# Performance work log

Measured on AMD Instinct MI355X. Metric: run time of the kernel, lower is better.

The kernel has to match this reference:

```python
import jax, jax.numpy as jnp
from jax import lax
import numpy as np

MAX_VAL = 255.0
LEVELS = 5
MS_WEIGHTS = np.array([0.0448, 0.2856, 0.3001, 0.2363, 0.1333], dtype=np.float32)


def _gaussian_window(window_size: int, sigma: float) -> jnp.ndarray:
    # 1D gaussian -> outer product -> [1, 1, ws, ws] conv kernel (channel=1 depthwise)
    x = np.arange(window_size, dtype=np.float64)
    g = np.exp(-((x - window_size // 2) ** 2) / (2.0 * sigma ** 2))
    g = (g / g.sum()).astype(np.float32)
    w2d = np.outer(g, g)
    return jnp.asarray(w2d[None, None, :, :])


def _conv_same(x, win, pad):
    return lax.conv_general_dilated(
        x, win, window_strides=(1, 1), padding=[(pad, pad), (pad, pad)],
        dimension_numbers=('NCHW', 'OIHW', 'NCHW'))


def _ssim_level(img1, img2):
    _, _, w, h = img1.shape
    window_size = min(w, h, 11)
    sigma = 1.5 * window_size / 11
    win = _gaussian_window(window_size, sigma)
    pad = window_size // 2

    mu1 = _conv_same(img1, win, pad)
    mu2 = _conv_same(img2, win, pad)
    mu1_sq = mu1 * mu1
    mu2_sq = mu2 * mu2
    mu1_mu2 = mu1 * mu2
    sigma1_sq = _conv_same(img1 * img1, win, pad) - mu1_sq
    sigma2_sq = _conv_same(img2 * img2, win, pad) - mu2_sq
    sigma12 = _conv_same(img1 * img2, win, pad) - mu1_mu2

    C1 = (0.01 * MAX_VAL) ** 2
    C2 = (0.03 * MAX_VAL) ** 2
    V1 = 2.0 * sigma12 + C2
    V2 = sigma1_sq + sigma2_sq + C2
    ssim_map = (2.0 * mu1_mu2 + C1) * V1 / ((mu1_sq + mu2_sq + C1) * V2)
    mcs_map = V1 / V2
    return ssim_map.mean(), mcs_map.mean()


def _avg_pool2(x):
    b, c, h, w = x.shape
    return x.reshape(b, c, h // 2, 2, w // 2, 2).mean(axis=(3, 5))


def _ms_ssim(img1, img2):
    msssim = []
    mcs = []
    for _ in range(LEVELS):
        s, m = _ssim_level(img1, img2)
        msssim.append(s)
        mcs.append(m)
        img1 = _avg_pool2(img1)
        img2 = _avg_pool2(img2)
    weight = jnp.asarray(MS_WEIGHTS)
    mcs = jnp.stack(mcs)
    value = jnp.prod(mcs[:LEVELS - 1] ** weight[:LEVELS - 1]) * msssim[-1] ** weight[LEVELS - 1]
    return jnp.clip(value / 2.0, 0.0, 1.0)


def setup_inputs() -> dict:
    key = jax.random.key(0)
    k1, k2 = jax.random.split(key)
    shape = (16, 1, 512, 512)
    img1 = jax.random.uniform(k1, shape, dtype=jnp.float32)
    img2 = jax.random.uniform(k2, shape, dtype=jnp.float32)
    return {"img1": img1, "img2": img2}


def reference(img1, img2):
    return _ms_ssim(img1, img2)
```

## Files before the change

kernel.cpp:

```cpp
#include <hip/hip_runtime.h>
#include <math.h>


#define WS 11
#define TW 64
#define TH 32
#define SROWS 42
#define HSTRIDE 68

__device__ __forceinline__ void gauss_weights(float* w) {
    float s = 0.f;
#pragma unroll
    for (int j = 0; j < WS; ++j) {
        float d = (float)(j - 5);
        float e = expf(-d * d / 4.5f);
        w[j] = e;
        s += e;
    }
    float inv = 1.f / s;
#pragma unroll
    for (int j = 0; j < WS; ++j) w[j] *= inv;
}

__global__ __launch_bounds__(256) void pool_all_kernel(
    const float* __restrict__ img1, const float* __restrict__ img2,
    float* __restrict__ l1a, float* __restrict__ l1b,
    float* __restrict__ l2a, float* __restrict__ l2b,
    float* __restrict__ l3a, float* __restrict__ l3b,
    float* __restrict__ l4a, float* __restrict__ l4b)
{
    __shared__ float buf[64 * 68];
    __shared__ float pl1[32 * 36];
    __shared__ float pl2[16 * 20];
    __shared__ float pl3[8 * 12];
    const int tid = threadIdx.x;
    const int rx = blockIdx.x, ry = blockIdx.y, b = blockIdx.z;
    const int gx0 = rx * 64, gy0 = ry * 64;

#pragma unroll 1
    for (int q = 0; q < 2; ++q) {
        const float* src = (q == 0 ? img1 : img2) + (size_t)b * 512 * 512;
        float* d1 = (q == 0 ? l1a : l1b) + (size_t)b * 256 * 256;
        float* d2 = (q == 0 ? l2a : l2b) + (size_t)b * 128 * 128;
        float* d3 = (q == 0 ? l3a : l3b) + (size_t)b * 64 * 64;
        float* d4 = (q == 0 ? l4a : l4b) + (size_t)b * 32 * 32;
        if (q) __syncthreads();
        for (int t = tid; t < 1024; t += 256) {
            int r = t >> 4, c4 = t & 15;
            float4 v = *(const float4*)(src + (size_t)(gy0 + r) * 512 + gx0 + 4 * c4);
            *(float4*)&buf[r * 68 + 4 * c4] = v;
        }
        __syncthreads();
        for (int t = tid; t < 1024; t += 256) {
            int r = t >> 5, c = t & 31;
            const float* p = &buf[(2 * r) * 68 + 2 * c];
            float v = 0.25f * ((p[0] + p[1]) + (p[68] + p[69]));
            pl1[r * 36 + c] = v;
            d1[(size_t)(32 * ry + r) * 256 + 32 * rx + c] = v;
        }
        __syncthreads();
        {
            int r = tid >> 4, c = tid & 15;
            const float* p = &pl1[(2 * r) * 36 + 2 * c];
            float v = 0.25f * ((p[0] + p[1]) + (p[36] + p[37]));
            pl2[r * 20 + c] = v;
            d2[(size_t)(16 * ry + r) * 128 + 16 * rx + c] = v;
        }
        __syncthreads();
        if (tid < 64) {
            int r = tid >> 3, c = tid & 7;
            const float* p = &pl2[(2 * r) * 20 + 2 * c];
            float v = 0.25f * ((p[0] + p[1]) + (p[20] + p[21]));
            pl3[r * 12 + c] = v;
            d3[(size_t)(8 * ry + r) * 64 + 8 * rx + c] = v;
        }
        __syncthreads();
        if (tid < 16) {
            int r = tid >> 2, c = tid & 3;
            const float* p = &pl3[(2 * r) * 12 + 2 * c];
            float v = 0.25f * ((p[0] + p[1]) + (p[12] + p[13]));
            d4[(size_t)(4 * ry + r) * 32 + 4 * rx + c] = v;
        }
    }
}

__global__ __launch_bounds__(256) void ssim_fused_kernel(
    const float* __restrict__ img1, const float* __restrict__ img2,
    const float* __restrict__ l1a, const float* __restrict__ l1b,
    const float* __restrict__ l2a, const float* __restrict__ l2b,
    const float* __restrict__ l3a, const float* __restrict__ l3b,
    const float* __restrict__ l4a, const float* __restrict__ l4b,
    float* __restrict__ partials)
{
    __shared__ float hS[SROWS * HSTRIDE];
    __shared__ float hD[SROWS * HSTRIDE];
    __shared__ float hS2[SROWS * HSTRIDE];
    __shared__ float hD2[SROWS * HSTRIDE];
    __shared__ float red[2][4];

    const int tid = threadIdx.x;
    const int lin = blockIdx.x;

    int level, base;
    if (lin < 2048)      { level = 0; base = 0; }
    else if (lin < 2560) { level = 1; base = 2048; }
    else if (lin < 2688) { level = 2; base = 2560; }
    else if (lin < 2720) { level = 3; base = 2688; }
    else                 { level = 4; base = 2720; }
    const int Wt[5]   = {512, 256, 128, 64, 32};
    const int ntxl[5] = {3, 2, 1, 0, 0};
    const int ntyl[5] = {4, 3, 2, 1, 0};
    const int W = Wt[level], H = W;
    const int li = lin - base;
    const int tx = li & ((1 << ntxl[level]) - 1);
    const int rem = li >> ntxl[level];
    const int ty = rem & ((1 << ntyl[level]) - 1);
    const int b = rem >> ntyl[level];

    const float* ip1; const float* ip2;
    if (level == 0)      { ip1 = img1; ip2 = img2; }
    else if (level == 1) { ip1 = l1a; ip2 = l1b; }
    else if (level == 2) { ip1 = l2a; ip2 = l2b; }
    else if (level == 3) { ip1 = l3a; ip2 = l3b; }
    else                 { ip1 = l4a; ip2 = l4b; }
    const float* p1 = ip1 + (size_t)b * H * W;
    const float* p2 = ip2 + (size_t)b * H * W;

    const int x0 = tx * TW, y0 = ty * TH;

    float w[WS];
    gauss_weights(w);

#pragma unroll 1
    for (int t = tid; t < SROWS * 16; t += 256) {
        int r = t >> 4, xg = t & 15;
        int gy = y0 - 5 + r;
        int gxb = x0 - 8 + 4 * xg;
        float fs[20], fd[20];
        if (gy >= 0 && gy < H) {
            const float* r1p = p1 + (size_t)gy * W;
            const float* r2p = p2 + (size_t)gy * W;
#pragma unroll
            for (int k = 0; k < 5; ++k) {
                int gx = gxb + 4 * k;
                float4 a = make_float4(0.f, 0.f, 0.f, 0.f);
                float4 c = make_float4(0.f, 0.f, 0.f, 0.f);
                if (gx >= 0 && gx + 3 < W) {
                    a = *(const float4*)(r1p + gx);
                    c = *(const float4*)(r2p + gx);
                } else if (gx + 3 >= 0 && gx < W) {
                    float t1[4] = {0.f, 0.f, 0.f, 0.f};
                    float t2[4] = {0.f, 0.f, 0.f, 0.f};
#pragma unroll
                    for (int u = 0; u < 4; ++u) {
                        int gxx = gx + u;
                        if (gxx >= 0 && gxx < W) { t1[u] = r1p[gxx]; t2[u] = r2p[gxx]; }
                    }
                    a = make_float4(t1[0], t1[1], t1[2], t1[3]);
                    c = make_float4(t2[0], t2[1], t2[2], t2[3]);
                }
                fs[4 * k]     = a.x + c.x;  fd[4 * k]     = a.x - c.x;
                fs[4 * k + 1] = a.y + c.y;  fd[4 * k + 1] = a.y - c.y;
                fs[4 * k + 2] = a.z + c.z;  fd[4 * k + 2] = a.z - c.z;
                fs[4 * k + 3] = a.w + c.w;  fd[4 * k + 3] = a.w - c.w;
            }
        } else {
#pragma unroll
            for (int k = 0; k < 20; ++k) { fs[k] = 0.f; fd[k] = 0.f; }
        }
        float qs[14], qd[14];
#pragma unroll
        for (int k = 0; k < 14; ++k) {
            qs[k] = fs[k + 3] * fs[k + 3];
            qd[k] = fd[k + 3] * fd[k + 3];
        }
        float oS[4], oD[4], oS2[4], oD2[4];
#pragma unroll
        for (int c = 0; c < 4; ++c) {
            float aS = 0.f, aD = 0.f, aS2 = 0.f, aD2 = 0.f;
#pragma unroll
            for (int j = 0; j < WS; ++j) {
                float wj = w[j];
                aS  = fmaf(wj, fs[3 + c + j], aS);
                aD  = fmaf(wj, fd[3 + c + j], aD);
                aS2 = fmaf(wj, qs[c + j], aS2);
                aD2 = fmaf(wj, qd[c + j], aD2);
            }
            oS[c] = aS; oD[c] = aD; oS2[c] = aS2; oD2[c] = aD2;
        }
        int ho = r * HSTRIDE + 4 * xg;
        *(float4*)&hS[ho]  = make_float4(oS[0], oS[1], oS[2], oS[3]);
        *(float4*)&hD[ho]  = make_float4(oD[0], oD[1], oD[2], oD[3]);
        *(float4*)&hS2[ho] = make_float4(oS2[0], oS2[1], oS2[2], oS2[3]);
        *(float4*)&hD2[ho] = make_float4(oD2[0], oD2[1], oD2[2], oD2[3]);
    }
    __syncthreads();

    const int x = tid & 15;
    const int g = tid >> 4;
    float accS[2][4], accD[2][4], accS2[2][4], accD2[2][4];
#pragma unroll
    for (int rr = 0; rr < 2; ++rr)
#pragma unroll
        for (int c = 0; c < 4; ++c) {
            accS[rr][c] = 0.f; accD[rr][c] = 0.f;
            accS2[rr][c] = 0.f; accD2[rr][c] = 0.f;
        }

#pragma unroll
    for (int r = 0; r < 12; ++r) {
        int ho = (2 * g + r) * HSTRIDE + 4 * x;
        float4 vS  = *(const float4*)&hS[ho];
        float4 vD  = *(const float4*)&hD[ho];
        float4 vS2 = *(const float4*)&hS2[ho];
        float4 vD2 = *(const float4*)&hD2[ho];
        float lS[4] = {vS.x, vS.y, vS.z, vS.w};
        float lD[4] = {vD.x, vD.y, vD.z, vD.w};
        float lS2[4] = {vS2.x, vS2.y, vS2.z, vS2.w};
        float lD2[4] = {vD2.x, vD2.y, vD2.z, vD2.w};
        if (r < 11) {
            float wv = w[r];
#pragma unroll
            for (int c = 0; c < 4; ++c) {
                accS[0][c]  = fmaf(wv, lS[c],  accS[0][c]);
                accD[0][c]  = fmaf(wv, lD[c],  accD[0][c]);
                accS2[0][c] = fmaf(wv, lS2[c], accS2[0][c]);
                accD2[0][c] = fmaf(wv, lD2[c], accD2[0][c]);
            }
        }
        if (r >= 1) {
            float wv = w[r - 1];
#pragma unroll
            for (int c = 0; c < 4; ++c) {
                accS[1][c]  = fmaf(wv, lS[c],  accS[1][c]);
                accD[1][c]  = fmaf(wv, lD[c],  accD[1][c]);
                accS2[1][c] = fmaf(wv, lS2[c], accS2[1][c]);
                accD2[1][c] = fmaf(wv, lD2[c], accD2[1][c]);
            }
        }
    }

    const float C1 = 6.5025f;
    const float C2 = 58.5225f;
    const int Hv = min(TH, H - y0);
    const int Wv = min(TW, W - x0);
    float sacc = 0.f, macc = 0.f;
#pragma unroll
    for (int rr = 0; rr < 2; ++rr) {
        int row = 2 * g + rr;
#pragma unroll
        for (int c = 0; c < 4; ++c) {
            float ms = accS[rr][c], md = accD[rr][c];
            float es = accS2[rr][c], ed = accD2[rr][c];
            float ms2 = ms * ms, md2 = md * md;
            float a  = 0.5f * (ms2 - md2);
            float bb = 0.5f * (ms2 + md2);
            float pq = 0.5f * (es - ed);
            float qq = 0.5f * (es + ed);
            float V1 = (pq - a) + C2;
            float V2 = (qq - bb) + C2;
            float num = a + C1;
            float den = bb + C1;
            float inv = 1.0f / (den * V2);
            float sv = num * V1 * inv;
            float mv = V1 * den * inv;
            if (row < Hv && (4 * x + c) < Wv) { sacc += sv; macc += mv; }
        }
    }

#pragma unroll
    for (int o = 32; o > 0; o >>= 1) {
        sacc += __shfl_down(sacc, o);
        macc += __shfl_down(macc, o);
    }
    int wave = tid >> 6, lane = tid & 63;
    if (lane == 0) { red[0][wave] = sacc; red[1][wave] = macc; }
    __syncthreads();
    if (tid == 0) {
        float s = red[0][0] + red[0][1] + red[0][2] + red[0][3];
        float m = red[1][0] + red[1][1] + red[1][2] + red[1][3];
        partials[2 * lin] = s;
        partials[2 * lin + 1] = m;
    }
}

__global__ __launch_bounds__(256) void finalize_kernel(
    const float* __restrict__ partials, float* __restrict__ out)
{
    __shared__ float lvl_s[5], lvl_m[5];
    __shared__ float red[2][4];
    const int nb[5] = {2048, 512, 128, 32, 16};
    const int off[5] = {0, 2048, 2560, 2688, 2720};
    const float npix[5] = {16.f * 512 * 512, 16.f * 256 * 256, 16.f * 128 * 128,
                           16.f * 64 * 64, 16.f * 32 * 32};
    const int tid = threadIdx.x;

    for (int l = 0; l < 5; ++l) {
        float s = 0.f, m = 0.f;
        for (int i = tid; i < nb[l]; i += 256) {
            s += partials[2 * (off[l] + i)];
            m += partials[2 * (off[l] + i) + 1];
        }
#pragma unroll
        for (int o = 32; o > 0; o >>= 1) {
            s += __shfl_down(s, o);
            m += __shfl_down(m, o);
        }
        int wave = tid >> 6, lane = tid & 63;
        if (lane == 0) { red[0][wave] = s; red[1][wave] = m; }
        __syncthreads();
        if (tid == 0) {
            lvl_s[l] = (red[0][0] + red[0][1] + red[0][2] + red[0][3]) / npix[l];
            lvl_m[l] = (red[1][0] + red[1][1] + red[1][2] + red[1][3]) / npix[l];
        }
        __syncthreads();
    }

    if (tid == 0) {
        const float w[5] = {0.0448f, 0.2856f, 0.3001f, 0.2363f, 0.1333f};
        float v = powf(lvl_m[0], w[0]) * powf(lvl_m[1], w[1]) * powf(lvl_m[2], w[2]) *
                  powf(lvl_m[3], w[3]) * powf(lvl_s[4], w[4]);
        v *= 0.5f;
        v = fminf(fmaxf(v, 0.f), 1.f);
        out[0] = v;
    }
}

extern "C" void kernel_launch(void* const* d_in, const int* in_sizes, int n_in,
                              void* d_out, int out_size, void* d_ws, size_t ws_size,
                              hipStream_t stream) {
    const float* img1 = (const float*)d_in[0];
    const float* img2 = (const float*)d_in[1];
    float* out = (float*)d_out;

    const int B = 16;

    float* wsf = (float*)d_ws;
    float* partials = wsf;
    float* p = wsf + 5472;
    float* l1a = p; p += (size_t)B * 256 * 256;
    float* l1b = p; p += (size_t)B * 256 * 256;
    float* l2a = p; p += (size_t)B * 128 * 128;
    float* l2b = p; p += (size_t)B * 128 * 128;
    float* l3a = p; p += (size_t)B * 64 * 64;
    float* l3b = p; p += (size_t)B * 64 * 64;
    float* l4a = p; p += (size_t)B * 32 * 32;
    float* l4b = p; p += (size_t)B * 32 * 32;

    dim3 block(256);

    pool_all_kernel<<<dim3(8, 8, B), block, 0, stream>>>(
        img1, img2, l1a, l1b, l2a, l2b, l3a, l3b, l4a, l4b);

    ssim_fused_kernel<<<dim3(2736), block, 0, stream>>>(
        img1, img2, l1a, l1b, l2a, l2b, l3a, l3b, l4a, l4b, partials);

    finalize_kernel<<<1, block, 0, stream>>>(partials, out);
}
```

Measured before the change: 129.4 us.

## Fuse image pyramid pooling into level-0 SSIM kernel and split remaining levels

Removes the standalone pooling kernel. The level-0 SSIM tile kernel now also computes the 2x2 average pools for levels 1–4 from its own 64x32 tile and writes them to global buffers. The remaining levels run in a separate kernel that reads those buffers. This avoids a second full pass over both input images and one launch, at the cost of more work and shared memory in the level-0 kernel. Levels 1–4 can no longer overlap with level 0, since they now run in a later launch.

```diff
diff --git a/kernel.cpp b/kernel.cpp
--- a/kernel.cpp
+++ b/kernel.cpp
@@ -22,114 +22,13 @@
     for (int j = 0; j < WS; ++j) w[j] *= inv;
 }
 
-__global__ __launch_bounds__(256) void pool_all_kernel(
-    const float* __restrict__ img1, const float* __restrict__ img2,
-    float* __restrict__ l1a, float* __restrict__ l1b,
-    float* __restrict__ l2a, float* __restrict__ l2b,
-    float* __restrict__ l3a, float* __restrict__ l3b,
-    float* __restrict__ l4a, float* __restrict__ l4b)
+__device__ __forceinline__ void ssim_tile(
+    const float* __restrict__ p1, const float* __restrict__ p2,
+    int H, int W, int x0, int y0, const float* w,
+    float* hS, float* hD, float* hS2, float* hD2,
+    float red[2][4], float* __restrict__ partials, int part_idx)
 {
-    __shared__ float buf[64 * 68];
-    __shared__ float pl1[32 * 36];
-    __shared__ float pl2[16 * 20];
-    __shared__ float pl3[8 * 12];
     const int tid = threadIdx.x;
-    const int rx = blockIdx.x, ry = blockIdx.y, b = blockIdx.z;
-    const int gx0 = rx * 64, gy0 = ry * 64;
-
-#pragma unroll 1
-    for (int q = 0; q < 2; ++q) {
-        const float* src = (q == 0 ? img1 : img2) + (size_t)b * 512 * 512;
-        float* d1 = (q == 0 ? l1a : l1b) + (size_t)b * 256 * 256;
-        float* d2 = (q == 0 ? l2a : l2b) + (size_t)b * 128 * 128;
-        float* d3 = (q == 0 ? l3a : l3b) + (size_t)b * 64 * 64;
-        float* d4 = (q == 0 ? l4a : l4b) + (size_t)b * 32 * 32;
-        if (q) __syncthreads();
-        for (int t = tid; t < 1024; t += 256) {
-            int r = t >> 4, c4 = t & 15;
-            float4 v = *(const float4*)(src + (size_t)(gy0 + r) * 512 + gx0 + 4 * c4);
-            *(float4*)&buf[r * 68 + 4 * c4] = v;
-        }
-        __syncthreads();
-        for (int t = tid; t < 1024; t += 256) {
-            int r = t >> 5, c = t & 31;
-            const float* p = &buf[(2 * r) * 68 + 2 * c];
-            float v = 0.25f * ((p[0] + p[1]) + (p[68] + p[69]));
-            pl1[r * 36 + c] = v;
-            d1[(size_t)(32 * ry + r) * 256 + 32 * rx + c] = v;
-        }
-        __syncthreads();
-        {
-            int r = tid >> 4, c = tid & 15;
-            const float* p = &pl1[(2 * r) * 36 + 2 * c];
-            float v = 0.25f * ((p[0] + p[1]) + (p[36] + p[37]));
-            pl2[r * 20 + c] = v;
-            d2[(size_t)(16 * ry + r) * 128 + 16 * rx + c] = v;
-        }
-        __syncthreads();
-        if (tid < 64) {
-            int r = tid >> 3, c = tid & 7;
-            const float* p = &pl2[(2 * r) * 20 + 2 * c];
-            float v = 0.25f * ((p[0] + p[1]) + (p[20] + p[21]));
-            pl3[r * 12 + c] = v;
-            d3[(size_t)(8 * ry + r) * 64 + 8 * rx + c] = v;
-        }
-        __syncthreads();
-        if (tid < 16) {
-            int r = tid >> 2, c = tid & 3;
-            const float* p = &pl3[(2 * r) * 12 + 2 * c];
-            float v = 0.25f * ((p[0] + p[1]) + (p[12] + p[13]));
-            d4[(size_t)(4 * ry + r) * 32 + 4 * rx + c] = v;
-        }
-    }
-}
-
-__global__ __launch_bounds__(256) void ssim_fused_kernel(
-    const float* __restrict__ img1, const float* __restrict__ img2,
-    const float* __restrict__ l1a, const float* __restrict__ l1b,
-    const float* __restrict__ l2a, const float* __restrict__ l2b,
-    const float* __restrict__ l3a, const float* __restrict__ l3b,
-    const float* __restrict__ l4a, const float* __restrict__ l4b,
-    float* __restrict__ partials)
-{
-    __shared__ float hS[SROWS * HSTRIDE];
-    __shared__ float hD[SROWS * HSTRIDE];
-    __shared__ float hS2[SROWS * HSTRIDE];
-    __shared__ float hD2[SROWS * HSTRIDE];
-    __shared__ float red[2][4];
-
-    const int tid = threadIdx.x;
-    const int lin = blockIdx.x;
-
-    int level, base;
-    if (lin < 2048)      { level = 0; base = 0; }
-    else if (lin < 2560) { level = 1; base = 2048; }
-    else if (lin < 2688) { level = 2; base = 2560; }
-    else if (lin < 2720) { level = 3; base = 2688; }
-    else                 { level = 4; base = 2720; }
-    const int Wt[5]   = {512, 256, 128, 64, 32};
-    const int ntxl[5] = {3, 2, 1, 0, 0};
-    const int ntyl[5] = {4, 3, 2, 1, 0};
-    const int W = Wt[level], H = W;
-    const int li = lin - base;
-    const int tx = li & ((1 << ntxl[level]) - 1);
-    const int rem = li >> ntxl[level];
-    const int ty = rem & ((1 << ntyl[level]) - 1);
-    const int b = rem >> ntyl[level];
-
-    const float* ip1; const float* ip2;
-    if (level == 0)      { ip1 = img1; ip2 = img2; }
-    else if (level == 1) { ip1 = l1a; ip2 = l1b; }
-    else if (level == 2) { ip1 = l2a; ip2 = l2b; }
-    else if (level == 3) { ip1 = l3a; ip2 = l3b; }
-    else                 { ip1 = l4a; ip2 = l4b; }
-    const float* p1 = ip1 + (size_t)b * H * W;
-    const float* p2 = ip2 + (size_t)b * H * W;
-
-    const int x0 = tx * TW, y0 = ty * TH;
-
-    float w[WS];
-    gauss_weights(w);
 
 #pragma unroll 1
     for (int t = tid; t < SROWS * 16; t += 256) {
@@ -279,9 +178,312 @@
     if (tid == 0) {
         float s = red[0][0] + red[0][1] + red[0][2] + red[0][3];
         float m = red[1][0] + red[1][1] + red[1][2] + red[1][3];
-        partials[2 * lin] = s;
-        partials[2 * lin + 1] = m;
-    }
+        partials[2 * part_idx] = s;
+        partials[2 * part_idx + 1] = m;
+    }
+}
+
+__global__ __launch_bounds__(256) void ssim_l0_pool_kernel(
+    const float* __restrict__ img1, const float* __restrict__ img2,
+    float* __restrict__ l1a, float* __restrict__ l1b,
+    float* __restrict__ l2a, float* __restrict__ l2b,
+    float* __restrict__ l3a, float* __restrict__ l3b,
+    float* __restrict__ l4a, float* __restrict__ l4b,
+    float* __restrict__ partials)
+{
+    __shared__ float hS[SROWS * HSTRIDE];
+    __shared__ float hD[SROWS * HSTRIDE];
+    __shared__ float hS2[SROWS * HSTRIDE];
+    __shared__ float hD2[SROWS * HSTRIDE];
+    __shared__ float pl1a[16 * 36];
+    __shared__ float pl1b[16 * 36];
+    __shared__ float red[2][4];
+
+    const int tid = threadIdx.x;
+    const int tx = blockIdx.x, ty = blockIdx.y, b = blockIdx.z;
+    const int x0 = tx * TW, y0 = ty * TH;
+    const float* p1 = img1 + (size_t)b * 512 * 512;
+    const float* p2 = img2 + (size_t)b * 512 * 512;
+
+    float w[WS];
+    gauss_weights(w);
+
+#pragma unroll 1
+    for (int t = tid; t < SROWS * 16; t += 256) {
+        int r = t >> 4, xg = t & 15;
+        int gy = y0 - 5 + r;
+        int gxb = x0 - 8 + 4 * xg;
+        float fs[20], fd[20];
+        if (gy >= 0 && gy < 512) {
+            const float* r1p = p1 + (size_t)gy * 512;
+            const float* r2p = p2 + (size_t)gy * 512;
+#pragma unroll
+            for (int k = 0; k < 5; ++k) {
+                int gx = gxb + 4 * k;
+                float4 a = make_float4(0.f, 0.f, 0.f, 0.f);
+                float4 c = make_float4(0.f, 0.f, 0.f, 0.f);
+                if (gx >= 0 && gx + 3 < 512) {
+                    a = *(const float4*)(r1p + gx);
+                    c = *(const float4*)(r2p + gx);
+                } else if (gx + 3 >= 0 && gx < 512) {
+                    float t1[4] = {0.f, 0.f, 0.f, 0.f};
+                    float t2[4] = {0.f, 0.f, 0.f, 0.f};
+#pragma unroll
+                    for (int u = 0; u < 4; ++u) {
+                        int gxx = gx + u;
+                        if (gxx >= 0 && gxx < 512) { t1[u] = r1p[gxx]; t2[u] = r2p[gxx]; }
+                    }
+                    a = make_float4(t1[0], t1[1], t1[2], t1[3]);
+                    c = make_float4(t2[0], t2[1], t2[2], t2[3]);
+                }
+                fs[4 * k]     = a.x + c.x;  fd[4 * k]     = a.x - c.x;
+                fs[4 * k + 1] = a.y + c.y;  fd[4 * k + 1] = a.y - c.y;
+                fs[4 * k + 2] = a.z + c.z;  fd[4 * k + 2] = a.z - c.z;
+                fs[4 * k + 3] = a.w + c.w;  fd[4 * k + 3] = a.w - c.w;
+            }
+        } else {
+#pragma unroll
+            for (int k = 0; k < 20; ++k) { fs[k] = 0.f; fd[k] = 0.f; }
+        }
+        float qs[14], qd[14];
+#pragma unroll
+        for (int k = 0; k < 14; ++k) {
+            qs[k] = fs[k + 3] * fs[k + 3];
+            qd[k] = fd[k + 3] * fd[k + 3];
+        }
+        float oS[4], oD[4], oS2[4], oD2[4];
+#pragma unroll
+        for (int c = 0; c < 4; ++c) {
+            float aS = 0.f, aD = 0.f, aS2 = 0.f, aD2 = 0.f;
+#pragma unroll
+            for (int j = 0; j < WS; ++j) {
+                float wj = w[j];
+                aS  = fmaf(wj, fs[3 + c + j], aS);
+                aD  = fmaf(wj, fd[3 + c + j], aD);
+                aS2 = fmaf(wj, qs[c + j], aS2);
+                aD2 = fmaf(wj, qd[c + j], aD2);
+            }
+            oS[c] = aS; oD[c] = aD; oS2[c] = aS2; oD2[c] = aD2;
+        }
+        int ho = r * HSTRIDE + 4 * xg;
+        *(float4*)&hS[ho]  = make_float4(oS[0], oS[1], oS[2], oS[3]);
+        *(float4*)&hD[ho]  = make_float4(oD[0], oD[1], oD[2], oD[3]);
+        *(float4*)&hS2[ho] = make_float4(oS2[0], oS2[1], oS2[2], oS2[3]);
+        *(float4*)&hD2[ho] = make_float4(oD2[0], oD2[1], oD2[2], oD2[3]);
+    }
+
+    for (int t = tid; t < 512; t += 256) {
+        int r = t >> 5, c = t & 31;
+        int gy = y0 + 2 * r, gx = x0 + 2 * c;
+        const float* a0 = p1 + (size_t)gy * 512 + gx;
+        const float* c0 = p2 + (size_t)gy * 512 + gx;
+        float2 u0 = *(const float2*)a0;
+        float2 u1 = *(const float2*)(a0 + 512);
+        float2 t0 = *(const float2*)c0;
+        float2 t1 = *(const float2*)(c0 + 512);
+        float v1 = 0.25f * ((u0.x + u0.y) + (u1.x + u1.y));
+        float v2 = 0.25f * ((t0.x + t0.y) + (t1.x + t1.y));
+        size_t o1 = (size_t)b * 256 * 256 + (size_t)(y0 / 2 + r) * 256 + (x0 / 2 + c);
+        l1a[o1] = v1;
+        l1b[o1] = v2;
+        pl1a[r * 36 + c] = v1;
+        pl1b[r * 36 + c] = v2;
+    }
+    __syncthreads();
+
+    if (tid < 64) {
+        int lane = tid;
+#pragma unroll
+        for (int t = lane; t < 128; t += 64) {
+            int r = t >> 4, c = t & 15;
+            int R = 2 * r, C = 2 * c;
+            float v1 = 0.25f * ((pl1a[R * 36 + C] + pl1a[R * 36 + C + 1]) +
+                                (pl1a[(R + 1) * 36 + C] + pl1a[(R + 1) * 36 + C + 1]));
+            float v2 = 0.25f * ((pl1b[R * 36 + C] + pl1b[R * 36 + C + 1]) +
+                                (pl1b[(R + 1) * 36 + C] + pl1b[(R + 1) * 36 + C + 1]));
+            size_t o = (size_t)b * 128 * 128 + (size_t)(y0 / 4 + r) * 128 + (x0 / 4 + c);
+            l2a[o] = v1;
+            l2b[o] = v2;
+        }
+        if (lane < 32) {
+            int r = lane >> 3, c = lane & 7;
+            float q1[2][2], q2[2][2];
+#pragma unroll
+            for (int i = 0; i < 2; ++i)
+#pragma unroll
+                for (int j = 0; j < 2; ++j) {
+                    int R = 4 * r + 2 * i, C = 4 * c + 2 * j;
+                    q1[i][j] = 0.25f * ((pl1a[R * 36 + C] + pl1a[R * 36 + C + 1]) +
+                                        (pl1a[(R + 1) * 36 + C] + pl1a[(R + 1) * 36 + C + 1]));
+                    q2[i][j] = 0.25f * ((pl1b[R * 36 + C] + pl1b[R * 36 + C + 1]) +
+                                        (pl1b[(R + 1) * 36 + C] + pl1b[(R + 1) * 36 + C + 1]));
+                }
+            float v1 = 0.25f * ((q1[0][0] + q1[0][1]) + (q1[1][0] + q1[1][1]));
+            float v2 = 0.25f * ((q2[0][0] + q2[0][1]) + (q2[1][0] + q2[1][1]));
+            size_t o = (size_t)b * 64 * 64 + (size_t)(y0 / 8 + r) * 64 + (x0 / 8 + c);
+            l3a[o] = v1;
+            l3b[o] = v2;
+        }
+        if (lane < 8) {
+            int r = lane >> 2, c = lane & 3;
+            float p3a[2][2], p3b[2][2];
+#pragma unroll
+            for (int i3 = 0; i3 < 2; ++i3)
+#pragma unroll
+                for (int j3 = 0; j3 < 2; ++j3) {
+                    float p2a[2][2], p2b[2][2];
+#pragma unroll
+                    for (int i2 = 0; i2 < 2; ++i2)
+#pragma unroll
+                        for (int j2 = 0; j2 < 2; ++j2) {
+                            int R = 8 * r + 4 * i3 + 2 * i2;
+                            int C = 8 * c + 4 * j3 + 2 * j2;
+                            p2a[i2][j2] = 0.25f * ((pl1a[R * 36 + C] + pl1a[R * 36 + C + 1]) +
+                                                   (pl1a[(R + 1) * 36 + C] + pl1a[(R + 1) * 36 + C + 1]));
+                            p2b[i2][j2] = 0.25f * ((pl1b[R * 36 + C] + pl1b[R * 36 + C + 1]) +
+                                                   (pl1b[(R + 1) * 36 + C] + pl1b[(R + 1) * 36 + C + 1]));
+                        }
+                    p3a[i3][j3] = 0.25f * ((p2a[0][0] + p2a[0][1]) + (p2a[1][0] + p2a[1][1]));
+                    p3b[i3][j3] = 0.25f * ((p2b[0][0] + p2b[0][1]) + (p2b[1][0] + p2b[1][1]));
+                }
+            float v1 = 0.25f * ((p3a[0][0] + p3a[0][1]) + (p3a[1][0] + p3a[1][1]));
+            float v2 = 0.25f * ((p3b[0][0] + p3b[0][1]) + (p3b[1][0] + p3b[1][1]));
+            size_t o = (size_t)b * 32 * 32 + (size_t)(y0 / 16 + r) * 32 + (x0 / 16 + c);
+            l4a[o] = v1;
+            l4b[o] = v2;
+        }
+    }
+
+    {
+        const int x = tid & 15;
+        const int g = tid >> 4;
+        float accS[2][4], accD[2][4], accS2[2][4], accD2[2][4];
+#pragma unroll
+        for (int rr = 0; rr < 2; ++rr)
+#pragma unroll
+            for (int c = 0; c < 4; ++c) {
+                accS[rr][c] = 0.f; accD[rr][c] = 0.f;
+                accS2[rr][c] = 0.f; accD2[rr][c] = 0.f;
+            }
+
+#pragma unroll
+        for (int r = 0; r < 12; ++r) {
+            int ho = (2 * g + r) * HSTRIDE + 4 * x;
+            float4 vS  = *(const float4*)&hS[ho];
+            float4 vD  = *(const float4*)&hD[ho];
+            float4 vS2 = *(const float4*)&hS2[ho];
+            float4 vD2 = *(const float4*)&hD2[ho];
+            float lS[4] = {vS.x, vS.y, vS.z, vS.w};
+            float lD[4] = {vD.x, vD.y, vD.z, vD.w};
+            float lS2[4] = {vS2.x, vS2.y, vS2.z, vS2.w};
+            float lD2[4] = {vD2.x, vD2.y, vD2.z, vD2.w};
+            if (r < 11) {
+                float wv = w[r];
+#pragma unroll
+                for (int c = 0; c < 4; ++c) {
+                    accS[0][c]  = fmaf(wv, lS[c],  accS[0][c]);
+                    accD[0][c]  = fmaf(wv, lD[c],  accD[0][c]);
+                    accS2[0][c] = fmaf(wv, lS2[c], accS2[0][c]);
+                    accD2[0][c] = fmaf(wv, lD2[c], accD2[0][c]);
+                }
+            }
+            if (r >= 1) {
+                float wv = w[r - 1];
+#pragma unroll
+                for (int c = 0; c < 4; ++c) {
+                    accS[1][c]  = fmaf(wv, lS[c],  accS[1][c]);
+                    accD[1][c]  = fmaf(wv, lD[c],  accD[1][c]);
+                    accS2[1][c] = fmaf(wv, lS2[c], accS2[1][c]);
+                    accD2[1][c] = fmaf(wv, lD2[c], accD2[1][c]);
+                }
+            }
+        }
+
+        const float C1 = 6.5025f;
+        const float C2 = 58.5225f;
+        float sacc = 0.f, macc = 0.f;
+#pragma unroll
+        for (int rr = 0; rr < 2; ++rr) {
+#pragma unroll
+            for (int c = 0; c < 4; ++c) {
+                float ms = accS[rr][c], md = accD[rr][c];
+                float es = accS2[rr][c], ed = accD2[rr][c];
+                float ms2 = ms * ms, md2 = md * md;
+                float a  = 0.5f * (ms2 - md2);
+                float bb = 0.5f * (ms2 + md2);
+                float pq = 0.5f * (es - ed);
+                float qq = 0.5f * (es + ed);
+                float V1 = (pq - a) + C2;
+                float V2 = (qq - bb) + C2;
+                float num = a + C1;
+                float den = bb + C1;
+                float inv = 1.0f / (den * V2);
+                sacc += num * V1 * inv;
+                macc += V1 * den * inv;
+            }
+        }
+
+#pragma unroll
+        for (int o = 32; o > 0; o >>= 1) {
+            sacc += __shfl_down(sacc, o);
+            macc += __shfl_down(macc, o);
+        }
+        int wave = tid >> 6, lane = tid & 63;
+        if (lane == 0) { red[0][wave] = sacc; red[1][wave] = macc; }
+        __syncthreads();
+        if (tid == 0) {
+            float s = red[0][0] + red[0][1] + red[0][2] + red[0][3];
+            float m = red[1][0] + red[1][1] + red[1][2] + red[1][3];
+            int linear = ((b * 16 + ty) * 8) + tx;
+            partials[2 * linear] = s;
+            partials[2 * linear + 1] = m;
+        }
+    }
+}
+
+__global__ __launch_bounds__(256) void ssim_rest_kernel(
+    const float* __restrict__ l1a, const float* __restrict__ l1b,
+    const float* __restrict__ l2a, const float* __restrict__ l2b,
+    const float* __restrict__ l3a, const float* __restrict__ l3b,
+    const float* __restrict__ l4a, const float* __restrict__ l4b,
+    float* __restrict__ partials)
+{
+    __shared__ float hS[SROWS * HSTRIDE];
+    __shared__ float hD[SROWS * HSTRIDE];
+    __shared__ float hS2[SROWS * HSTRIDE];
+    __shared__ float hD2[SROWS * HSTRIDE];
+    __shared__ float red[2][4];
+
+    const int lin = blockIdx.x;
+    int level, base;
+    if (lin < 512)      { level = 1; base = 0; }
+    else if (lin < 640) { level = 2; base = 512; }
+    else if (lin < 672) { level = 3; base = 640; }
+    else                { level = 4; base = 672; }
+    const int Wt[4]   = {256, 128, 64, 32};
+    const int ntxl[4] = {2, 1, 0, 0};
+    const int ntyl[4] = {3, 2, 1, 0};
+    const int idx = level - 1;
+    const int W = Wt[idx], H = W;
+    const int li = lin - base;
+    const int tx = li & ((1 << ntxl[idx]) - 1);
+    const int rem = li >> ntxl[idx];
+    const int ty = rem & ((1 << ntyl[idx]) - 1);
+    const int b = rem >> ntyl[idx];
+
+    const float* ip1; const float* ip2;
+    if (level == 1)      { ip1 = l1a; ip2 = l1b; }
+    else if (level == 2) { ip1 = l2a; ip2 = l2b; }
+    else if (level == 3) { ip1 = l3a; ip2 = l3b; }
+    else                 { ip1 = l4a; ip2 = l4b; }
+    const float* p1 = ip1 + (size_t)b * H * W;
+    const float* p2 = ip2 + (size_t)b * H * W;
+
+    float w[WS];
+    gauss_weights(w);
+
+    ssim_tile(p1, p2, H, W, tx * TW, ty * TH, w, hS, hD, hS2, hD2, red,
+              partials, lin);
 }
 
 __global__ __launch_bounds__(256) void finalize_kernel(
@@ -349,11 +551,11 @@
 
     dim3 block(256);
 
-    pool_all_kernel<<<dim3(8, 8, B), block, 0, stream>>>(
-        img1, img2, l1a, l1b, l2a, l2b, l3a, l3b, l4a, l4b);
-
-    ssim_fused_kernel<<<dim3(2736), block, 0, stream>>>(
+    ssim_l0_pool_kernel<<<dim3(8, 16, B), block, 0, stream>>>(
         img1, img2, l1a, l1b, l2a, l2b, l3a, l3b, l4a, l4b, partials);
+
+    ssim_rest_kernel<<<dim3(688), block, 0, stream>>>(
+        l1a, l1b, l2a, l2b, l3a, l3b, l4a, l4b, partials + 2 * 2048);
 
     finalize_kernel<<<1, block, 0, stream>>>(partials, out);
 }
```

Measured after the change: 124.6 us. -3.8%, faster.

## Split fused SSIM into separate horizontal and vertical passes with fp16 intermediates

Applied to the files above, without the earlier changes.

Replaces the single shared-memory tiled SSIM kernel with two kernels. The horizontal pass writes blurred sum/difference and their squares to global memory as packed half2. The vertical pass reads them back and computes the SSIM/CS partial sums. This removes the halo recomputation and LDS staging of the fused tile, but adds a global round trip of intermediates plus an extra launch. Storing intermediates in fp16 loses precision, and values around 2*255 squared could overflow half range, so the output may be wrong.

```diff
diff --git a/kernel.cpp b/kernel.cpp
--- a/kernel.cpp
+++ b/kernel.cpp
@@ -1,12 +1,9 @@
 #include <hip/hip_runtime.h>
+#include <hip/hip_fp16.h>
 #include <math.h>
 
 
 #define WS 11
-#define TW 64
-#define TH 32
-#define SROWS 42
-#define HSTRIDE 68
 
 __device__ __forceinline__ void gauss_weights(float* w) {
     float s = 0.f;
@@ -20,6 +17,19 @@
     float inv = 1.f / s;
 #pragma unroll
     for (int j = 0; j < WS; ++j) w[j] *= inv;
+}
+
+__device__ __forceinline__ void decode_lvl(
+    int lin, int& level, int& b, int& pbase, int& W, int& lw, size_t& poff)
+{
+    int li, bl;
+    if (lin < 4096)      { level = 0; li = lin;        bl = 8; W = 512; lw = 9; poff = 0; }
+    else if (lin < 5120) { level = 1; li = lin - 4096; bl = 6; W = 256; lw = 8; poff = 4194304; }
+    else if (lin < 5376) { level = 2; li = lin - 5120; bl = 4; W = 128; lw = 7; poff = 5242880; }
+    else if (lin < 5440) { level = 3; li = lin - 5376; bl = 2; W = 64;  lw = 6; poff = 5505024; }
+    else                 { level = 4; li = lin - 5440; bl = 0; W = 32;  lw = 5; poff = 5570560; }
+    b = li >> bl;
+    pbase = (li - (b << bl)) << 10;
 }
 
 __global__ __launch_bounds__(256) void pool_all_kernel(
@@ -84,38 +94,18 @@
     }
 }
 
-__global__ __launch_bounds__(256) void ssim_fused_kernel(
+__global__ __launch_bounds__(256) void h_kernel(
     const float* __restrict__ img1, const float* __restrict__ img2,
     const float* __restrict__ l1a, const float* __restrict__ l1b,
     const float* __restrict__ l2a, const float* __restrict__ l2b,
     const float* __restrict__ l3a, const float* __restrict__ l3b,
     const float* __restrict__ l4a, const float* __restrict__ l4b,
-    float* __restrict__ partials)
-{
-    __shared__ float hS[SROWS * HSTRIDE];
-    __shared__ float hD[SROWS * HSTRIDE];
-    __shared__ float hS2[SROWS * HSTRIDE];
-    __shared__ float hD2[SROWS * HSTRIDE];
-    __shared__ float red[2][4];
-
+    __half2* __restrict__ pSD, __half2* __restrict__ pQ)
+{
     const int tid = threadIdx.x;
     const int lin = blockIdx.x;
-
-    int level, base;
-    if (lin < 2048)      { level = 0; base = 0; }
-    else if (lin < 2560) { level = 1; base = 2048; }
-    else if (lin < 2688) { level = 2; base = 2560; }
-    else if (lin < 2720) { level = 3; base = 2688; }
-    else                 { level = 4; base = 2720; }
-    const int Wt[5]   = {512, 256, 128, 64, 32};
-    const int ntxl[5] = {3, 2, 1, 0, 0};
-    const int ntyl[5] = {4, 3, 2, 1, 0};
-    const int W = Wt[level], H = W;
-    const int li = lin - base;
-    const int tx = li & ((1 << ntxl[level]) - 1);
-    const int rem = li >> ntxl[level];
-    const int ty = rem & ((1 << ntyl[level]) - 1);
-    const int b = rem >> ntyl[level];
+    int level, b, pbase, W, lw; size_t poff;
+    decode_lvl(lin, level, b, pbase, W, lw, poff);
 
     const float* ip1; const float* ip2;
     if (level == 0)      { ip1 = img1; ip2 = img2; }
@@ -123,149 +113,137 @@
     else if (level == 2) { ip1 = l2a; ip2 = l2b; }
     else if (level == 3) { ip1 = l3a; ip2 = l3b; }
     else                 { ip1 = l4a; ip2 = l4b; }
-    const float* p1 = ip1 + (size_t)b * H * W;
-    const float* p2 = ip2 + (size_t)b * H * W;
-
-    const int x0 = tx * TW, y0 = ty * TH;
+    ip1 += (size_t)b * W * W;
+    ip2 += (size_t)b * W * W;
 
     float w[WS];
     gauss_weights(w);
 
-#pragma unroll 1
-    for (int t = tid; t < SROWS * 16; t += 256) {
-        int r = t >> 4, xg = t & 15;
-        int gy = y0 - 5 + r;
-        int gxb = x0 - 8 + 4 * xg;
-        float fs[20], fd[20];
-        if (gy >= 0 && gy < H) {
-            const float* r1p = p1 + (size_t)gy * W;
-            const float* r2p = p2 + (size_t)gy * W;
-#pragma unroll
-            for (int k = 0; k < 5; ++k) {
-                int gx = gxb + 4 * k;
-                float4 a = make_float4(0.f, 0.f, 0.f, 0.f);
-                float4 c = make_float4(0.f, 0.f, 0.f, 0.f);
-                if (gx >= 0 && gx + 3 < W) {
-                    a = *(const float4*)(r1p + gx);
-                    c = *(const float4*)(r2p + gx);
-                } else if (gx + 3 >= 0 && gx < W) {
-                    float t1[4] = {0.f, 0.f, 0.f, 0.f};
-                    float t2[4] = {0.f, 0.f, 0.f, 0.f};
-#pragma unroll
-                    for (int u = 0; u < 4; ++u) {
-                        int gxx = gx + u;
-                        if (gxx >= 0 && gxx < W) { t1[u] = r1p[gxx]; t2[u] = r2p[gxx]; }
-                    }
-                    a = make_float4(t1[0], t1[1], t1[2], t1[3]);
-                    c = make_float4(t2[0], t2[1], t2[2], t2[3]);
-                }
-                fs[4 * k]     = a.x + c.x;  fd[4 * k]     = a.x - c.x;
-                fs[4 * k + 1] = a.y + c.y;  fd[4 * k + 1] = a.y - c.y;
-                fs[4 * k + 2] = a.z + c.z;  fd[4 * k + 2] = a.z - c.z;
-                fs[4 * k + 3] = a.w + c.w;  fd[4 * k + 3] = a.w - c.w;
+    const int p = pbase + tid * 4;
+    const int row = p >> lw;
+    const int col = p - (row << lw);
+
+    const float* r1 = ip1 + (size_t)row * W;
+    const float* r2 = ip2 + (size_t)row * W;
+
+    float f1[20], f2[20];
+    if (col >= 8 && col + 12 <= W) {
+#pragma unroll
+        for (int k = 0; k < 5; ++k) {
+            float4 a = *(const float4*)(r1 + col - 8 + 4 * k);
+            float4 c = *(const float4*)(r2 + col - 8 + 4 * k);
+            f1[4 * k] = a.x; f1[4 * k + 1] = a.y; f1[4 * k + 2] = a.z; f1[4 * k + 3] = a.w;
+            f2[4 * k] = c.x; f2[4 * k + 1] = c.y; f2[4 * k + 2] = c.z; f2[4 * k + 3] = c.w;
+        }
+    } else {
+#pragma unroll
+        for (int k = 0; k < 5; ++k) {
+#pragma unroll
+            for (int u = 0; u < 4; ++u) {
+                int gx = col - 8 + 4 * k + u;
+                bool ok = (gx >= 0) && (gx < W);
+                f1[4 * k + u] = ok ? r1[gx] : 0.f;
+                f2[4 * k + u] = ok ? r2[gx] : 0.f;
             }
-        } else {
-#pragma unroll
-            for (int k = 0; k < 20; ++k) { fs[k] = 0.f; fd[k] = 0.f; }
-        }
-        float qs[14], qd[14];
-#pragma unroll
-        for (int k = 0; k < 14; ++k) {
-            qs[k] = fs[k + 3] * fs[k + 3];
-            qd[k] = fd[k + 3] * fd[k + 3];
-        }
-        float oS[4], oD[4], oS2[4], oD2[4];
-#pragma unroll
-        for (int c = 0; c < 4; ++c) {
-            float aS = 0.f, aD = 0.f, aS2 = 0.f, aD2 = 0.f;
-#pragma unroll
-            for (int j = 0; j < WS; ++j) {
-                float wj = w[j];
-                aS  = fmaf(wj, fs[3 + c + j], aS);
-                aD  = fmaf(wj, fd[3 + c + j], aD);
-                aS2 = fmaf(wj, qs[c + j], aS2);
-                aD2 = fmaf(wj, qd[c + j], aD2);
-            }
-            oS[c] = aS; oD[c] = aD; oS2[c] = aS2; oD2[c] = aD2;
-        }
-        int ho = r * HSTRIDE + 4 * xg;
-        *(float4*)&hS[ho]  = make_float4(oS[0], oS[1], oS[2], oS[3]);
-        *(float4*)&hD[ho]  = make_float4(oD[0], oD[1], oD[2], oD[3]);
-        *(float4*)&hS2[ho] = make_float4(oS2[0], oS2[1], oS2[2], oS2[3]);
-        *(float4*)&hD2[ho] = make_float4(oD2[0], oD2[1], oD2[2], oD2[3]);
-    }
-    __syncthreads();
-
-    const int x = tid & 15;
-    const int g = tid >> 4;
-    float accS[2][4], accD[2][4], accS2[2][4], accD2[2][4];
-#pragma unroll
-    for (int rr = 0; rr < 2; ++rr)
-#pragma unroll
-        for (int c = 0; c < 4; ++c) {
-            accS[rr][c] = 0.f; accD[rr][c] = 0.f;
-            accS2[rr][c] = 0.f; accD2[rr][c] = 0.f;
-        }
-
-#pragma unroll
-    for (int r = 0; r < 12; ++r) {
-        int ho = (2 * g + r) * HSTRIDE + 4 * x;
-        float4 vS  = *(const float4*)&hS[ho];
-        float4 vD  = *(const float4*)&hD[ho];
-        float4 vS2 = *(const float4*)&hS2[ho];
-        float4 vD2 = *(const float4*)&hD2[ho];
-        float lS[4] = {vS.x, vS.y, vS.z, vS.w};
-        float lD[4] = {vD.x, vD.y, vD.z, vD.w};
-        float lS2[4] = {vS2.x, vS2.y, vS2.z, vS2.w};
-        float lD2[4] = {vD2.x, vD2.y, vD2.z, vD2.w};
-        if (r < 11) {
-            float wv = w[r];
+        }
+    }
+
+    float fs[20], fd[20];
+#pragma unroll
+    for (int k = 0; k < 20; ++k) {
+        fs[k] = f1[k] + f2[k];
+        fd[k] = f1[k] - f2[k];
+    }
+    float qs[14], qd[14];
+#pragma unroll
+    for (int k = 0; k < 14; ++k) {
+        qs[k] = fs[k + 3] * fs[k + 3];
+        qd[k] = fd[k + 3] * fd[k + 3];
+    }
+    __half2 outSD[4], outQ[4];
+#pragma unroll
+    for (int c = 0; c < 4; ++c) {
+        float aS = 0.f, aD = 0.f, aS2 = 0.f, aD2 = 0.f;
+#pragma unroll
+        for (int j = 0; j < WS; ++j) {
+            float wj = w[j];
+            aS  = fmaf(wj, fs[3 + c + j], aS);
+            aD  = fmaf(wj, fd[3 + c + j], aD);
+            aS2 = fmaf(wj, qs[c + j], aS2);
+            aD2 = fmaf(wj, qd[c + j], aD2);
+        }
+        outSD[c] = __float22half2_rn(make_float2(aS, aD));
+        outQ[c]  = __float22half2_rn(make_float2(aS2, aD2));
+    }
+    size_t op = poff + (size_t)b * W * W + p;
+    *(float4*)&pSD[op] = *(const float4*)outSD;
+    *(float4*)&pQ[op]  = *(const float4*)outQ;
+}
+
+__global__ __launch_bounds__(256) void v_kernel(
+    const __half2* __restrict__ pSD, const __half2* __restrict__ pQ,
+    float* __restrict__ partials)
+{
+    __shared__ float red[2][4];
+    const int tid = threadIdx.x;
+    const int lin = blockIdx.x;
+    int level, b, pbase, W, lw; size_t poff;
+    decode_lvl(lin, level, b, pbase, W, lw, poff);
+
+    float w[WS];
+    gauss_weights(w);
+
+    const int p = pbase + tid * 4;
+    const int row = p >> lw;
+    const int col = p - (row << lw);
+    const size_t ibase = poff + (size_t)b * W * W;
+
+    float aS[4] = {0.f, 0.f, 0.f, 0.f};
+    float aD[4] = {0.f, 0.f, 0.f, 0.f};
+    float aS2[4] = {0.f, 0.f, 0.f, 0.f};
+    float aD2[4] = {0.f, 0.f, 0.f, 0.f};
+
+#pragma unroll
+    for (int j = 0; j < WS; ++j) {
+        int r = row - 5 + j;
+        if ((unsigned)r < (unsigned)W) {
+            size_t off = ibase + ((size_t)r << lw) + col;
+            float4 rawSD = *(const float4*)&pSD[off];
+            float4 rawQ  = *(const float4*)&pQ[off];
+            const __half2* hsd = (const __half2*)&rawSD;
+            const __half2* hq  = (const __half2*)&rawQ;
+            float wv = w[j];
 #pragma unroll
             for (int c = 0; c < 4; ++c) {
-                accS[0][c]  = fmaf(wv, lS[c],  accS[0][c]);
-                accD[0][c]  = fmaf(wv, lD[c],  accD[0][c]);
-                accS2[0][c] = fmaf(wv, lS2[c], accS2[0][c]);
-                accD2[0][c] = fmaf(wv, lD2[c], accD2[0][c]);
-            }
-        }
-        if (r >= 1) {
-            float wv = w[r - 1];
-#pragma unroll
-            for (int c = 0; c < 4; ++c) {
-                accS[1][c]  = fmaf(wv, lS[c],  accS[1][c]);
-                accD[1][c]  = fmaf(wv, lD[c],  accD[1][c]);
-                accS2[1][c] = fmaf(wv, lS2[c], accS2[1][c]);
-                accD2[1][c] = fmaf(wv, lD2[c], accD2[1][c]);
+                float2 sd = __half22float2(hsd[c]);
+                float2 q  = __half22float2(hq[c]);
+                aS[c]  = fmaf(wv, sd.x, aS[c]);
+                aD[c]  = fmaf(wv, sd.y, aD[c]);
+                aS2[c] = fmaf(wv, q.x,  aS2[c]);
+                aD2[c] = fmaf(wv, q.y,  aD2[c]);
             }
         }
     }
 
     const float C1 = 6.5025f;
     const float C2 = 58.5225f;
-    const int Hv = min(TH, H - y0);
-    const int Wv = min(TW, W - x0);
     float sacc = 0.f, macc = 0.f;
 #pragma unroll
-    for (int rr = 0; rr < 2; ++rr) {
-        int row = 2 * g + rr;
-#pragma unroll
-        for (int c = 0; c < 4; ++c) {
-            float ms = accS[rr][c], md = accD[rr][c];
-            float es = accS2[rr][c], ed = accD2[rr][c];
-            float ms2 = ms * ms, md2 = md * md;
-            float a  = 0.5f * (ms2 - md2);
-            float bb = 0.5f * (ms2 + md2);
-            float pq = 0.5f * (es - ed);
-            float qq = 0.5f * (es + ed);
-            float V1 = (pq - a) + C2;
-            float V2 = (qq - bb) + C2;
-            float num = a + C1;
-            float den = bb + C1;
-            float inv = 1.0f / (den * V2);
-            float sv = num * V1 * inv;
-            float mv = V1 * den * inv;
-            if (row < Hv && (4 * x + c) < Wv) { sacc += sv; macc += mv; }
-        }
+    for (int c = 0; c < 4; ++c) {
+        float ms = aS[c], md = aD[c];
+        float es = aS2[c], ed = aD2[c];
+        float ms2 = ms * ms, md2 = md * md;
+        float a  = 0.5f * (ms2 - md2);
+        float bb = 0.5f * (ms2 + md2);
+        float pq = 0.5f * (es - ed);
+        float qq = 0.5f * (es + ed);
+        float V1 = (pq - a) + C2;
+        float V2 = (qq - bb) + C2;
+        float num = a + C1;
+        float den = bb + C1;
+        float inv = 1.0f / (den * V2);
+        sacc += num * V1 * inv;
+        macc += V1 * den * inv;
     }
 
 #pragma unroll
@@ -289,8 +267,8 @@
 {
     __shared__ float lvl_s[5], lvl_m[5];
     __shared__ float red[2][4];
-    const int nb[5] = {2048, 512, 128, 32, 16};
-    const int off[5] = {0, 2048, 2560, 2688, 2720};
+    const int nb[5] = {4096, 1024, 256, 64, 16};
+    const int off[5] = {0, 4096, 5120, 5376, 5440};
     const float npix[5] = {16.f * 512 * 512, 16.f * 256 * 256, 16.f * 128 * 128,
                            16.f * 64 * 64, 16.f * 32 * 32};
     const int tid = threadIdx.x;
@@ -337,7 +315,7 @@
 
     float* wsf = (float*)d_ws;
     float* partials = wsf;
-    float* p = wsf + 5472;
+    float* p = wsf + 10912;
     float* l1a = p; p += (size_t)B * 256 * 256;
     float* l1b = p; p += (size_t)B * 256 * 256;
     float* l2a = p; p += (size_t)B * 128 * 128;
@@ -346,14 +324,18 @@
     float* l3b = p; p += (size_t)B * 64 * 64;
     float* l4a = p; p += (size_t)B * 32 * 32;
     float* l4b = p; p += (size_t)B * 32 * 32;
+    __half2* pSD = (__half2*)p;
+    __half2* pQ  = pSD + 5587456;
 
     dim3 block(256);
 
     pool_all_kernel<<<dim3(8, 8, B), block, 0, stream>>>(
         img1, img2, l1a, l1b, l2a, l2b, l3a, l3b, l4a, l4b);
 
-    ssim_fused_kernel<<<dim3(2736), block, 0, stream>>>(
-        img1, img2, l1a, l1b, l2a, l2b, l3a, l3b, l4a, l4b, partials);
+    h_kernel<<<dim3(5456), block, 0, stream>>>(
+        img1, img2, l1a, l1b, l2a, l2b, l3a, l3b, l4a, l4b, pSD, pQ);
+
+    v_kernel<<<dim3(5456), block, 0, stream>>>(pSD, pQ, partials);
 
     finalize_kernel<<<1, block, 0, stream>>>(partials, out);
 }
```

New measurement: 144.8 us. 11.8% more time.
